# Performance work log

Measured on AMD Instinct MI355X. Metric: run time of the kernel, lower is better.

Reference implementation:

```python
import jax, jax.numpy as jnp
import numpy as np

B, S, D = 256, 512, 768
SEP_ID = 2
BOS_ID = 0
PAD_ID = 1


def setup_inputs() -> dict:
    key = jax.random.key(0)
    k_h, = jax.random.split(key, 1)
    hidden_states = jax.random.normal(k_h, (B, S, D), dtype=jnp.float32)

    rng = np.random.default_rng(0)
    ids = rng.integers(5, 64000, size=(B, S), dtype=np.int64)
    mask = np.zeros((B, S), dtype=np.int64)
    title_len = rng.integers(3, 60, size=B)
    lead_len = rng.integers(10, 300, size=B)
    for i in range(B):
        tl, ll = int(title_len[i]), int(lead_len[i])
        ids[i, 0] = BOS_ID
        ids[i, 1 + tl] = SEP_ID          # first </s>
        ids[i, 2 + tl] = SEP_ID          # second </s>
        lead_end = 3 + tl + ll           # position of third </s>
        lead_end = min(lead_end, S - 1)
        ids[i, 3 + tl:lead_end] = rng.integers(5, 64000, size=lead_end - (3 + tl))
        ids[i, lead_end] = SEP_ID        # third </s>
        ids[i, lead_end + 1:] = PAD_ID
        mask[i, :lead_end + 1] = 1
    return {
        "hidden_states": hidden_states,
        "input_ids": jnp.asarray(ids),
        "attention_mask": jnp.asarray(mask),
        "sep_token_id": SEP_ID,
    }


def reference(hidden_states, input_ids, attention_mask, sep_token_id):
    Bsz, Slen, _ = hidden_states.shape
    idx = jnp.arange(Slen)
    sep = input_ids == sep_token_id                     # [B,S] bool
    cnt = jnp.cumsum(sep.astype(jnp.int32), axis=1)     # running sep count

    def kth_sep_pos(k):
        # position of k-th sep token; Slen sentinel if absent
        return jnp.min(jnp.where(sep & (cnt == k), idx[None, :], Slen), axis=1)

    pos1, pos2, pos3 = kth_sep_pos(1), kth_sep_pos(2), kth_sep_pos(3)
    nsep = sep.sum(axis=1)
    attn_len = attention_mask.sum(axis=1).astype(jnp.int32)

    title_end = pos1                                   # title = tokens [1, title_end)
    lead_start = pos2 + 1
    lead_end = jnp.where(nsep >= 3, pos3, attn_len)    # lead = tokens [lead_start, lead_end)

    tmask = (idx[None, :] >= 1) & (idx[None, :] < title_end[:, None])
    lmask = (idx[None, :] >= lead_start[:, None]) & (idx[None, :] < lead_end[:, None])

    def masked_mean(m):
        mf = m.astype(hidden_states.dtype)
        n = mf.sum(axis=1)                             # [B]
        s = jnp.einsum('bs,bsd->bd', mf, hidden_states)
        return s / jnp.maximum(n, 1.0)[:, None], n

    tmean, tn = masked_mean(tmask)
    lmean, ln = masked_mean(lmask)

    cls = hidden_states[:, 0, :]
    valid = nsep >= 2
    title_pool = jnp.where((valid & (tn > 0))[:, None], tmean, cls)
    lead_pool = jnp.where((valid & (ln > 0))[:, None], lmean, cls)
    return title_pool, lead_pool
```

## Files before the change

kernel.cpp:

```cpp
#include <hip/hip_runtime.h>

#define BATCH 256
#define SEQ   512
#define DIM   768
#define D4    192
#define NW    8
#define NTHR  (NW * 64)
#define ZCH   3

__global__ __launch_bounds__(NTHR) void seg_pool_fused(
    const float* __restrict__ hidden,
    const int*  __restrict__ ids,
    const int*  __restrict__ amask,
    const int*  __restrict__ sep_tok,
    float* __restrict__ out)
{
    const int b    = blockIdx.x;
    const int z    = blockIdx.y;
    const int seg  = blockIdx.z;
    const int t    = threadIdx.x;
    const int w    = t >> 6;
    const int lane = t & 63;

    __shared__ unsigned long long s_msep[NW];
    __shared__ int    s_att[NW];
    __shared__ int    s_info[3];
    __shared__ float4 s_red[NW][64];

    {
        const int id = ids[b * SEQ + t];
        const unsigned long long m = __ballot(id == sep_tok[0]);
        if (lane == 0) s_msep[w] = m;
    }
    __syncthreads();

    if (t == 0) {
        int nsep = 0, p0 = SEQ, p1 = SEQ, p2 = SEQ;
        #pragma unroll
        for (int c = 0; c < NW; ++c) {
            unsigned long long mm = s_msep[c];
            while (mm) {
                const int bit = __ffsll((long long)mm) - 1;
                const int pos = c * 64 + bit;
                if (nsep == 0)      p0 = pos;
                else if (nsep == 1) p1 = pos;
                else if (nsep == 2) p2 = pos;
                ++nsep;
                mm &= mm - 1;
            }
        }
        const bool valid = (nsep >= 2);
        if (seg == 1) {
            int n = p0 - 1;
            if (n < 0 || !valid) n = 0;
            s_info[0] = 1; s_info[1] = n; s_info[2] = 0;
        } else if (nsep >= 3) {
            int n = p2 - (p1 + 1);
            if (n < 0) n = 0;
            s_info[0] = p1 + 1; s_info[1] = n; s_info[2] = 0;
        } else {
            s_info[0] = p1 + 1;
            s_info[1] = valid ? -1 : 0;
            s_info[2] = valid ? 1 : 0;
        }
    }
    __syncthreads();

    if (s_info[2]) {
        const int am = amask[b * SEQ + t];
        const unsigned long long ma = __ballot(am != 0);
        if (lane == 0) s_att[w] = __popcll(ma);
        __syncthreads();
        if (t == 0) {
            int attn = 0;
            #pragma unroll
            for (int c = 0; c < NW; ++c) attn += s_att[c];
            int n = attn - s_info[0];
            if (n < 0) n = 0;
            s_info[1] = n;
        }
        __syncthreads();
    }

    const int start = s_info[0];
    const int n     = s_info[1];
    const int d4    = z * 64 + lane;

    const float4* __restrict__ h4 = (const float4*)hidden;
    const size_t base = (size_t)b * (SEQ * D4);

    const int chunk = (n + NW - 1) / NW;
    const int s0    = start + w * chunk;
    int s1          = s0 + chunk;
    const int send  = start + n;
    if (s1 > send) s1 = send;

    float4 acc = {0.f, 0.f, 0.f, 0.f};
    #pragma unroll 16
    for (int s = s0; s < s1; ++s) {
        const float4 v = h4[base + (size_t)s * D4 + d4];
        acc.x += v.x; acc.y += v.y; acc.z += v.z; acc.w += v.w;
    }
    s_red[w][lane] = acc;
    __syncthreads();

    if (t < 64) {
        float4 res;
        if (n > 0) {
            float4 a = {0.f, 0.f, 0.f, 0.f};
            #pragma unroll
            for (int c = 0; c < NW; ++c) {
                const float4 v = s_red[c][t];
                a.x += v.x; a.y += v.y; a.z += v.z; a.w += v.w;
            }
            const float fn = (float)n;
            res.x = a.x / fn; res.y = a.y / fn;
            res.z = a.z / fn; res.w = a.w / fn;
        } else {
            res = h4[base + d4];
        }
        const int seg_out = 1 - seg;
        float4* __restrict__ o4 = (float4*)out;
        o4[(size_t)seg_out * (BATCH * D4) + (size_t)b * D4 + d4] = res;
    }
}

extern "C" void kernel_launch(void* const* d_in, const int* in_sizes, int n_in,
                              void* d_out, int out_size, void* d_ws, size_t ws_size,
                              hipStream_t stream) {
    const float* hidden  = (const float*)d_in[0];
    const int*   ids     = (const int*)d_in[1];
    const int*   amask   = (const int*)d_in[2];
    const int*   sep_tok = (const int*)d_in[3];
    float*       out     = (float*)d_out;

    seg_pool_fused<<<dim3(BATCH, ZCH, 2), dim3(NTHR), 0, stream>>>(
        hidden, ids, amask, sep_tok, out);
}
```

Measured before the change: 30.39 us.

## Merge D-chunk blocks into one block per segment with 12 waves striding rows

Removes the grid dimension that split the 768-wide feature dimension into three blocks. Each block now covers a full row with 12 waves, and each wave interleaves across rows with stride 12 while accumulating three float4 columns per lane. This cuts the redundant sep-scan and attention-mask work that was repeated in every block, and gives each thread more independent loads in flight. In exchange there are a third as many blocks (512), which may reduce parallelism across the GPU, and the block size grows to 768 threads.

```diff
diff --git a/kernel.cpp b/kernel.cpp
--- a/kernel.cpp
+++ b/kernel.cpp
@@ -4,9 +4,8 @@
 #define SEQ   512
 #define DIM   768
 #define D4    192
-#define NW    8
-#define NTHR  (NW * 64)
-#define ZCH   3
+#define NWV   12
+#define NTHR  (NWV * 64)
 
 __global__ __launch_bounds__(NTHR) void seg_pool_fused(
     const float* __restrict__ hidden,
@@ -16,18 +15,17 @@
     float* __restrict__ out)
 {
     const int b    = blockIdx.x;
-    const int z    = blockIdx.y;
-    const int seg  = blockIdx.z;
+    const int seg  = blockIdx.y;
     const int t    = threadIdx.x;
     const int w    = t >> 6;
     const int lane = t & 63;
 
-    __shared__ unsigned long long s_msep[NW];
-    __shared__ int    s_att[NW];
+    __shared__ unsigned long long s_msep[8];
+    __shared__ int    s_att[8];
     __shared__ int    s_info[3];
-    __shared__ float4 s_red[NW][64];
+    __shared__ float4 s_red[NWV][D4];
 
-    {
+    if (t < SEQ) {
         const int id = ids[b * SEQ + t];
         const unsigned long long m = __ballot(id == sep_tok[0]);
         if (lane == 0) s_msep[w] = m;
@@ -37,7 +35,7 @@
     if (t == 0) {
         int nsep = 0, p0 = SEQ, p1 = SEQ, p2 = SEQ;
         #pragma unroll
-        for (int c = 0; c < NW; ++c) {
+        for (int c = 0; c < 8; ++c) {
             unsigned long long mm = s_msep[c];
             while (mm) {
                 const int bit = __ffsll((long long)mm) - 1;
@@ -60,21 +58,23 @@
             s_info[0] = p1 + 1; s_info[1] = n; s_info[2] = 0;
         } else {
             s_info[0] = p1 + 1;
-            s_info[1] = valid ? -1 : 0;
+            s_info[1] = 0;
             s_info[2] = valid ? 1 : 0;
         }
     }
     __syncthreads();
 
     if (s_info[2]) {
-        const int am = amask[b * SEQ + t];
-        const unsigned long long ma = __ballot(am != 0);
-        if (lane == 0) s_att[w] = __popcll(ma);
+        if (t < SEQ) {
+            const int am = amask[b * SEQ + t];
+            const unsigned long long ma = __ballot(am != 0);
+            if (lane == 0) s_att[w] = __popcll(ma);
+        }
         __syncthreads();
         if (t == 0) {
             int attn = 0;
             #pragma unroll
-            for (int c = 0; c < NW; ++c) attn += s_att[c];
+            for (int c = 0; c < 8; ++c) attn += s_att[c];
             int n = attn - s_info[0];
             if (n < 0) n = 0;
             s_info[1] = n;
@@ -84,32 +84,37 @@
 
     const int start = s_info[0];
     const int n     = s_info[1];
-    const int d4    = z * 64 + lane;
 
     const float4* __restrict__ h4 = (const float4*)hidden;
     const size_t base = (size_t)b * (SEQ * D4);
 
-    const int chunk = (n + NW - 1) / NW;
-    const int s0    = start + w * chunk;
-    int s1          = s0 + chunk;
-    const int send  = start + n;
-    if (s1 > send) s1 = send;
+    float4 a0 = {0.f, 0.f, 0.f, 0.f};
+    float4 a1 = {0.f, 0.f, 0.f, 0.f};
+    float4 a2 = {0.f, 0.f, 0.f, 0.f};
 
-    float4 acc = {0.f, 0.f, 0.f, 0.f};
-    #pragma unroll 16
-    for (int s = s0; s < s1; ++s) {
-        const float4 v = h4[base + (size_t)s * D4 + d4];
-        acc.x += v.x; acc.y += v.y; acc.z += v.z; acc.w += v.w;
+    const int nr = (n > w) ? (n - w + NWV - 1) / NWV : 0;
+    int s = start + w;
+    #pragma unroll 4
+    for (int k = 0; k < nr; ++k, s += NWV) {
+        const float4* __restrict__ r = h4 + base + (size_t)s * D4;
+        const float4 v0 = r[lane];
+        const float4 v1 = r[lane + 64];
+        const float4 v2 = r[lane + 128];
+        a0.x += v0.x; a0.y += v0.y; a0.z += v0.z; a0.w += v0.w;
+        a1.x += v1.x; a1.y += v1.y; a1.z += v1.z; a1.w += v1.w;
+        a2.x += v2.x; a2.y += v2.y; a2.z += v2.z; a2.w += v2.w;
     }
-    s_red[w][lane] = acc;
+    s_red[w][lane]       = a0;
+    s_red[w][lane + 64]  = a1;
+    s_red[w][lane + 128] = a2;
     __syncthreads();
 
-    if (t < 64) {
+    if (t < D4) {
         float4 res;
         if (n > 0) {
             float4 a = {0.f, 0.f, 0.f, 0.f};
             #pragma unroll
-            for (int c = 0; c < NW; ++c) {
+            for (int c = 0; c < NWV; ++c) {
                 const float4 v = s_red[c][t];
                 a.x += v.x; a.y += v.y; a.z += v.z; a.w += v.w;
             }
@@ -117,11 +122,11 @@
             res.x = a.x / fn; res.y = a.y / fn;
             res.z = a.z / fn; res.w = a.w / fn;
         } else {
-            res = h4[base + d4];
+            res = h4[base + t];
         }
         const int seg_out = 1 - seg;
         float4* __restrict__ o4 = (float4*)out;
-        o4[(size_t)seg_out * (BATCH * D4) + (size_t)b * D4 + d4] = res;
+        o4[(size_t)seg_out * (BATCH * D4) + (size_t)b * D4 + t] = res;
     }
 }
 
@@ -134,6 +139,6 @@
     const int*   sep_tok = (const int*)d_in[3];
     float*       out     = (float*)d_out;
 
-    seg_pool_fused<<<dim3(BATCH, ZCH, 2), dim3(NTHR), 0, stream>>>(
+    seg_pool_fused<<<dim3(BATCH, 2), dim3(NTHR), 0, stream>>>(
         hidden, ids, amask, sep_tok, out);
 }
```

Result: no change. 30.11 us (-0.9%).
